# Performance work log

Hardware: AMD Instinct MI355X
Metric: run time of the kernel (lower is better)

Reference implementation:

```python
import jax, jax.numpy as jnp
import numpy as np

B, D, H, C = 128, 512, 1024, 1000


def setup_inputs() -> dict:
    key = jax.random.key(0)
    k1, k2, k3 = jax.random.split(key, 3)
    x = jax.random.normal(k1, (B, D), dtype=jnp.float32)
    W1 = jax.random.normal(k2, (D, H), dtype=jnp.float32) * (1.0 / np.sqrt(D))
    b1 = jnp.zeros((H,), dtype=jnp.float32)
    W2 = jax.random.normal(k3, (H, C), dtype=jnp.float32) * (1.0 / np.sqrt(H))
    b2 = jnp.zeros((C,), dtype=jnp.float32)
    return {"x": x, "W1": W1, "b1": b1, "W2": W2, "b2": b2, "step": 0}


def _logits(W1, b1, W2, b2, xi):
    # 2-layer MLP forward for a single sample xi: [D] -> [C]
    h = jnp.maximum(xi @ W1 + b1, 0.0)
    return h @ W2 + b2


def _per_sample_loss(params, xi, key):
    W1, b1, W2, b2 = params
    logit = _logits(W1, b1, W2, b2, xi)  # [C]
    # model samples a label from its own softmax (multinomial); sampling is
    # non-differentiable, matching torch's multinomial -> stop_gradient
    y = jax.random.categorical(key, jax.lax.stop_gradient(logit))
    return -jax.nn.log_softmax(logit)[y]  # CrossEntropyLoss on 1 sample


def reference(x, W1, b1, W2, b2, step):
    params = (W1, b1, W2, b2)
    keys = jax.random.split(jax.random.key(42), x.shape[0])
    # vmap(grad(loss)) -> per-sample gradients for every parameter
    grads = jax.vmap(jax.grad(_per_sample_loss), in_axes=(None, 0, 0))(params, x, keys)
    n = jnp.asarray(x.shape[0], dtype=x.dtype)
    # trace_p = sum_b ||g_b||^2 / B for each parameter
    traces = [jnp.sum(g * g) / n for g in grads]
    overall = traces[0] + traces[1] + traces[2] + traces[3]
    return jnp.stack([overall] + traces)  # [5]: overall, W1, b1, W2, b2
```

## Files before the change

kernel.cpp:

```cpp
#include <hip/hip_runtime.h>
#include <hip/hip_bf16.h>
#include <stdint.h>
#include <math.h>

#define B_N 128
#define D_N 512
#define H_N 1024
#define C_N 1000
#define CP  1024
#define NPART 16
#define BH (B_N * H_N)

__device__ __forceinline__ uint32_t rotl32(uint32_t v, int r) {
  return (v << r) | (v >> (32 - r));
}

__device__ __forceinline__ void threefry2x32(uint32_t k0, uint32_t k1,
                                             uint32_t x0, uint32_t x1,
                                             uint32_t &o0, uint32_t &o1) {
  uint32_t ks2 = k0 ^ k1 ^ 0x1BD11BDAu;
#define TF_R(r) { x0 += x1; x1 = rotl32(x1, r); x1 ^= x0; }
  x0 += k0; x1 += k1;
  TF_R(13) TF_R(15) TF_R(26) TF_R(6)
  x0 += k1; x1 += ks2 + 1u;
  TF_R(17) TF_R(29) TF_R(16) TF_R(24)
  x0 += ks2; x1 += k0 + 2u;
  TF_R(13) TF_R(15) TF_R(26) TF_R(6)
  x0 += k0; x1 += k1 + 3u;
  TF_R(17) TF_R(29) TF_R(16) TF_R(24)
  x0 += k1; x1 += ks2 + 4u;
  TF_R(13) TF_R(15) TF_R(26) TF_R(6)
  x0 += ks2; x1 += k0 + 5u;
#undef TF_R
  o0 = x0; o1 = x1;
}

__device__ __forceinline__ float gumbel_from_key(uint32_t k0, uint32_t k1, uint32_t i) {
  uint32_t o0, o1;
  threefry2x32(k0, k1, 0u, i, o0, o1);
  uint32_t bits = o0 ^ o1;
  uint32_t fb = (bits >> 9) | 0x3f800000u;
  float f = __uint_as_float(fb) - 1.0f;
  const float tiny = 1.1754943508222875e-38f;
  float u = fmaxf(tiny, f * (1.0f - tiny) + tiny);
  return -logf(-logf(u));
}

__device__ __forceinline__ float block_sum512(float v, float* red) {
  #pragma unroll
  for (int o = 32; o; o >>= 1) v += __shfl_xor(v, o);
  __syncthreads();
  if ((threadIdx.x & 63) == 0) red[threadIdx.x >> 6] = v;
  __syncthreads();
  return red[0] + red[1] + red[2] + red[3] + red[4] + red[5] + red[6] + red[7];
}

__device__ __forceinline__ float block_max512(float v, float* red) {
  #pragma unroll
  for (int o = 32; o; o >>= 1) v = fmaxf(v, __shfl_xor(v, o));
  __syncthreads();
  if ((threadIdx.x & 63) == 0) red[threadIdx.x >> 6] = v;
  __syncthreads();
  float m = red[0];
  #pragma unroll
  for (int w = 1; w < 8; w++) m = fmaxf(m, red[w]);
  return m;
}

__device__ __forceinline__ void fma4(float4 &a, const float4 &b, float s) {
  a.x += b.x * s; a.y += b.y * s; a.z += b.z * s; a.w += b.w * s;
}

__global__ __launch_bounds__(256) void k_fc1(const float* __restrict__ X,
                                             const float* __restrict__ W1,
                                             float* __restrict__ hpart) {
  __shared__ float xT[32 * 20];
  int cbase = blockIdx.x * 256;
  int sbase = blockIdx.y * 16;
  int dz = blockIdx.z;
  int t = threadIdx.x;
  {
    int s = t >> 4;
    int d2 = (t & 15) * 2;
    float2 xv = *reinterpret_cast<const float2*>(
        &X[(sbase + s) * D_N + dz * 32 + d2]);
    xT[(d2 + 0) * 20 + s] = xv.x;
    xT[(d2 + 1) * 20 + s] = xv.y;
  }
  __syncthreads();
  int c4 = cbase + (t & 63) * 4;
  int s4 = (t >> 6) * 4;
  float4 acc0 = {0,0,0,0}, acc1 = {0,0,0,0}, acc2 = {0,0,0,0}, acc3 = {0,0,0,0};
  const float* W1p = W1 + (size_t)(dz * 32) * H_N + c4;
  float4 wb[4], wn[4];
  #pragma unroll
  for (int i = 0; i < 4; i++)
    wb[i] = *reinterpret_cast<const float4*>(W1p + i * H_N);
  for (int j0 = 0; j0 < 32; j0 += 4) {
    #pragma unroll
    for (int i = 0; i < 4; i++) {
      int jn = j0 + 4 + i; jn = (jn < 32) ? jn : 31;
      wn[i] = *reinterpret_cast<const float4*>(W1p + jn * H_N);
    }
    #pragma unroll
    for (int i = 0; i < 4; i++) {
      float4 xv = *reinterpret_cast<const float4*>(&xT[(j0 + i) * 20 + s4]);
      fma4(acc0, wb[i], xv.x);
      fma4(acc1, wb[i], xv.y);
      fma4(acc2, wb[i], xv.z);
      fma4(acc3, wb[i], xv.w);
    }
    #pragma unroll
    for (int i = 0; i < 4; i++) wb[i] = wn[i];
  }
  float* hp = hpart + (size_t)dz * BH;
  *reinterpret_cast<float4*>(&hp[(sbase + s4 + 0) * H_N + c4]) = acc0;
  *reinterpret_cast<float4*>(&hp[(sbase + s4 + 1) * H_N + c4]) = acc1;
  *reinterpret_cast<float4*>(&hp[(sbase + s4 + 2) * H_N + c4]) = acc2;
  *reinterpret_cast<float4*>(&hp[(sbase + s4 + 3) * H_N + c4]) = acc3;
}

__global__ __launch_bounds__(256) void k_fc2(const float* __restrict__ hpart,
                                             const float* __restrict__ b1,
                                             const float* __restrict__ W2,
                                             float* __restrict__ lpart) {
  __shared__ float hT[64 * 20];
  int cbase = blockIdx.x * 256;
  int sbase = blockIdx.y * 16;
  int kb = blockIdx.z;
  int jbase = kb * 64;
  int t = threadIdx.x;
  #pragma unroll
  for (int k = 0; k < 4; k++) {
    int idx = t + k * 256;
    int s = idx >> 6, j = idx & 63;
    float v = b1[jbase + j];
    #pragma unroll
    for (int p = 0; p < NPART; p++)
      v += hpart[(size_t)p * BH + (sbase + s) * H_N + jbase + j];
    hT[j * 20 + s] = fmaxf(v, 0.0f);
  }
  __syncthreads();
  int c4 = cbase + (t & 63) * 4;
  int s4 = (t >> 6) * 4;
  if (c4 < C_N) {
    float4 acc0 = {0,0,0,0}, acc1 = {0,0,0,0}, acc2 = {0,0,0,0}, acc3 = {0,0,0,0};
    const float* W2p = W2 + (size_t)jbase * C_N + c4;
    float4 wb[4], wn[4];
    #pragma unroll
    for (int i = 0; i < 4; i++)
      wb[i] = *reinterpret_cast<const float4*>(W2p + (size_t)i * C_N);
    for (int j0 = 0; j0 < 64; j0 += 4) {
      #pragma unroll
      for (int i = 0; i < 4; i++) {
        int jn = j0 + 4 + i; jn = (jn < 64) ? jn : 63;
        wn[i] = *reinterpret_cast<const float4*>(W2p + (size_t)jn * C_N);
      }
      #pragma unroll
      for (int i = 0; i < 4; i++) {
        float4 xv = *reinterpret_cast<const float4*>(&hT[(j0 + i) * 20 + s4]);
        fma4(acc0, wb[i], xv.x);
        fma4(acc1, wb[i], xv.y);
        fma4(acc2, wb[i], xv.z);
        fma4(acc3, wb[i], xv.w);
      }
      #pragma unroll
      for (int i = 0; i < 4; i++) wb[i] = wn[i];
    }
    float* lp = lpart + (size_t)kb * (B_N * CP);
    *reinterpret_cast<float4*>(&lp[(sbase + s4 + 0) * CP + c4]) = acc0;
    *reinterpret_cast<float4*>(&lp[(sbase + s4 + 1) * CP + c4]) = acc1;
    *reinterpret_cast<float4*>(&lp[(sbase + s4 + 2) * CP + c4]) = acc2;
    *reinterpret_cast<float4*>(&lp[(sbase + s4 + 3) * CP + c4]) = acc3;
  }
}

__global__ __launch_bounds__(512) void k_sample(const float* __restrict__ X,
                                                const float* __restrict__ hpart,
                                                const float* __restrict__ b1,
                                                const float* __restrict__ lpart,
                                                const float* __restrict__ b2,
                                                float* __restrict__ g,
                                                float* __restrict__ hfinal,
                                                float* __restrict__ xsq_out,
                                                float* __restrict__ samp_part) {
  __shared__ float lg[C_N];
  __shared__ float red[8];
  __shared__ float redv[8];
  __shared__ int   redi[8];
  __shared__ uint32_t keys[2];
  int b = blockIdx.x;
  int t = threadIdx.x;

  {
    float sA = b2[t];
    float sB = (t + 512 < C_N) ? b2[t + 512] : 0.f;
    #pragma unroll
    for (int p = 0; p < NPART; p++) {
      const float* lp = lpart + (size_t)p * (B_N * CP) + b * CP;
      sA += lp[t];
      if (t + 512 < C_N) sB += lp[t + 512];
    }
    lg[t] = sA;
    if (t + 512 < C_N) lg[t + 512] = sB;
  }
  if (t == 0) {
    uint32_t o0, o1;
    threefry2x32(0u, 42u, 0u, (uint32_t)b, o0, o1);
    keys[0] = o0; keys[1] = o1;
  }
  __syncthreads();
  uint32_t k0 = keys[0], k1 = keys[1];

  float bz = -INFINITY; int bi = 0x7fffffff;
  {
    float z0 = lg[t] + gumbel_from_key(k0, k1, (uint32_t)t);
    bz = z0; bi = t;
    if (t + 512 < C_N) {
      float z1 = lg[t + 512] + gumbel_from_key(k0, k1, (uint32_t)(t + 512));
      if (z1 > bz || (z1 == bz && (t + 512) < bi)) { bz = z1; bi = t + 512; }
    }
  }
  #pragma unroll
  for (int o = 32; o; o >>= 1) {
    float ov = __shfl_xor(bz, o);
    int   oi = __shfl_xor(bi, o);
    if (ov > bz || (ov == bz && oi < bi)) { bz = ov; bi = oi; }
  }
  if ((t & 63) == 0) { redv[t >> 6] = bz; redi[t >> 6] = bi; }
  __syncthreads();
  if (t == 0) {
    #pragma unroll
    for (int w = 1; w < 8; w++) {
      if (redv[w] > redv[0] || (redv[w] == redv[0] && redi[w] < redi[0])) {
        redv[0] = redv[w]; redi[0] = redi[w];
      }
    }
  }
  __syncthreads();
  int y = redi[0];

  float lm = lg[t];
  if (t + 512 < C_N) lm = fmaxf(lm, lg[t + 512]);
  float m = block_max512(lm, red);
  float ea = expf(lg[t] - m);
  float eb = (t + 512 < C_N) ? expf(lg[t + 512] - m) : 0.0f;
  float sum1 = block_sum512(ea + eb, red);
  float inv = 1.0f / sum1;

  float ga  = ea * inv - ((t == y) ? 1.0f : 0.0f);
  float gb2 = eb * inv - (((t + 512) == y) ? 1.0f : 0.0f);
  g[b * CP + t] = ga;
  g[b * CP + t + 512] = (t + 512 < C_N) ? gb2 : 0.0f;
  float gn = ga * ga + ((t + 512 < C_N) ? gb2 * gb2 : 0.0f);
  float tnorm = block_sum512(gn, red);

  float h0 = b1[t];
  float h1 = b1[t + 512];
  #pragma unroll
  for (int p = 0; p < NPART; p++) {
    const float* hp = hpart + (size_t)p * BH + b * H_N;
    h0 += hp[t];
    h1 += hp[t + 512];
  }
  hfinal[b * H_N + t] = h0;
  hfinal[b * H_N + t + 512] = h1;
  float r0 = fmaxf(h0, 0.f), r1 = fmaxf(h1, 0.f);
  float hsq = block_sum512(r0 * r0 + r1 * r1, red);

  float xv = (t < D_N) ? X[b * D_N + t] : 0.0f;
  float xsq = block_sum512(xv * xv, red);

  if (t == 0) {
    xsq_out[b] = xsq;
    samp_part[b * 2 + 0] = hsq * tnorm;
    samp_part[b * 2 + 1] = tnorm;
  }
}

__global__ __launch_bounds__(512) void k_bwd1(const float* __restrict__ g,
                                              const float* __restrict__ W2,
                                              const float* __restrict__ hfinal,
                                              const float* __restrict__ xsq,
                                              float* __restrict__ bwd_part) {
  __shared__ float gs[8 * 1024];
  __shared__ float xq[8];
  __shared__ float wred[8][2];
  int jb = blockIdx.x * 16;
  int sbase = blockIdx.y * 8;
  int t = threadIdx.x;
  #pragma unroll
  for (int k = 0; k < 16; k++) {
    int idx = t + k * 512;
    gs[idx] = g[(sbase + (idx >> 10)) * CP + (idx & 1023)];
  }
  if (t < 8) xq[t] = xsq[sbase + t];
  __syncthreads();

  int w = t >> 6, lane = t & 63;
  int j0 = jb + w * 2, j1 = j0 + 1;
  float a0[8] = {0,0,0,0,0,0,0,0};
  float a1[8] = {0,0,0,0,0,0,0,0};
  const float* w2r0 = W2 + (size_t)j0 * C_N;
  const float* w2r1 = W2 + (size_t)j1 * C_N;
  #pragma unroll
  for (int it = 0; it < 4; it++) {
    int c0 = it * 256 + lane * 4;
    bool act = (c0 < C_N);
    float4 wv0 = act ? *reinterpret_cast<const float4*>(w2r0 + c0)
                     : make_float4(0.f, 0.f, 0.f, 0.f);
    float4 wv1 = act ? *reinterpret_cast<const float4*>(w2r1 + c0)
                     : make_float4(0.f, 0.f, 0.f, 0.f);
    #pragma unroll
    for (int s = 0; s < 8; s++) {
      float4 gv = *reinterpret_cast<const float4*>(&gs[s * 1024 + c0]);
      a0[s] += wv0.x * gv.x + wv0.y * gv.y + wv0.z * gv.z + wv0.w * gv.w;
      a1[s] += wv1.x * gv.x + wv1.y * gv.y + wv1.z * gv.z + wv1.w * gv.w;
    }
  }
  #pragma unroll
  for (int off = 32; off; off >>= 1) {
    #pragma unroll
    for (int s = 0; s < 8; s++) {
      a0[s] += __shfl_xor(a0[s], off);
      a1[s] += __shfl_xor(a1[s], off);
    }
  }
  float cb = 0.f, cw = 0.f;
  #pragma unroll
  for (int s = 0; s < 8; s++) {
    float h0 = hfinal[(sbase + s) * H_N + j0];
    float h1 = hfinal[(sbase + s) * H_N + j1];
    float v0 = (h0 > 0.f) ? a0[s] : 0.f;
    float v1 = (h1 > 0.f) ? a1[s] : 0.f;
    float q = v0 * v0 + v1 * v1;
    cb += q;
    cw += xq[s] * q;
  }
  if (lane == 0) { wred[w][0] = cw; wred[w][1] = cb; }
  __syncthreads();
  if (t == 0) {
    float sw = 0.f, sb = 0.f;
    #pragma unroll
    for (int i = 0; i < 8; i++) { sw += wred[i][0]; sb += wred[i][1]; }
    int bid = blockIdx.y * 64 + blockIdx.x;
    bwd_part[bid * 2 + 0] = sw;
    bwd_part[bid * 2 + 1] = sb;
  }
}

__global__ __launch_bounds__(512) void k_final(const float* __restrict__ samp_part,
                                               const float* __restrict__ bwd_part,
                                               float* __restrict__ out) {
  __shared__ float red[8];
  int t = threadIdx.x;
  float w1v = bwd_part[t * 2 + 0] + bwd_part[(t + 512) * 2 + 0];
  float b1v = bwd_part[t * 2 + 1] + bwd_part[(t + 512) * 2 + 1];
  float w2v = (t < B_N) ? samp_part[t * 2 + 0] : 0.f;
  float b2v = (t < B_N) ? samp_part[t * 2 + 1] : 0.f;
  w1v = block_sum512(w1v, red);
  b1v = block_sum512(b1v, red);
  w2v = block_sum512(w2v, red);
  b2v = block_sum512(b2v, red);
  if (t == 0) {
    w1v /= 128.0f; b1v /= 128.0f; w2v /= 128.0f; b2v /= 128.0f;
    out[0] = w1v + b1v + w2v + b2v;
    out[1] = w1v;
    out[2] = b1v;
    out[3] = w2v;
    out[4] = b2v;
  }
}

extern "C" void kernel_launch(void* const* d_in, const int* in_sizes, int n_in,
                              void* d_out, int out_size, void* d_ws, size_t ws_size,
                              hipStream_t stream) {
  const float* X  = (const float*)d_in[0];
  const float* W1 = (const float*)d_in[1];
  const float* b1 = (const float*)d_in[2];
  const float* W2 = (const float*)d_in[3];
  const float* b2 = (const float*)d_in[4];
  float* out = (float*)d_out;

  float* ws        = (float*)d_ws;
  float* hpart     = ws;
  float* lpart     = hpart + NPART * BH;
  float* g         = lpart + NPART * (B_N*CP);
  float* hfinal    = g + (B_N * CP);
  float* xsq       = hfinal + BH;
  float* samp_part = xsq + 128;
  float* bwd_part  = samp_part + 256;

  k_fc1<<<dim3(4, 8, NPART), 256, 0, stream>>>(X, W1, hpart);
  k_fc2<<<dim3(4, 8, NPART), 256, 0, stream>>>(hpart, b1, W2, lpart);
  k_sample<<<B_N, 512, 0, stream>>>(X, hpart, b1, lpart, b2, g, hfinal, xsq, samp_part);
  k_bwd1<<<dim3(64, 16), 512, 0, stream>>>(g, W2, hfinal, xsq, bwd_part);
  k_final<<<1, 512, 0, stream>>>(samp_part, bwd_part, out);
}
```

Measured before the change: 57.68 us.

## Fuse all five stages into one cooperative persistent kernel with grid syncs

```diff
diff --git a/kernel.cpp b/kernel.cpp
--- a/kernel.cpp
+++ b/kernel.cpp
@@ -1,7 +1,10 @@
 #include <hip/hip_runtime.h>
+#include <hip/hip_cooperative_groups.h>
 #include <hip/hip_bf16.h>
 #include <stdint.h>
 #include <math.h>
+
+namespace cg = cooperative_groups;
 
 #define B_N 128
 #define D_N 512
@@ -71,6 +74,314 @@
   a.x += b.x * s; a.y += b.y * s; a.z += b.z * s; a.w += b.w * s;
 }
 
+union SMem {
+  struct { float xT[2][32 * 20]; } a;
+  struct { float hT[2][64 * 20]; } c;
+  struct { float lg[1024]; float red[8]; float redv[8];
+           int redi[8]; uint32_t keys[2]; } d;
+  struct { float gs[8 * 1024]; float xq[8];
+           float wred[8][2]; } e;
+};
+
+__global__ __launch_bounds__(512) void k_fused(
+    const float* __restrict__ X,  const float* __restrict__ W1,
+    const float* __restrict__ b1, const float* __restrict__ W2,
+    const float* __restrict__ b2,
+    float* __restrict__ hpart, float* __restrict__ lpart,
+    float* __restrict__ g, float* __restrict__ hfinal,
+    float* __restrict__ xsq_out, float* __restrict__ samp_part,
+    float* __restrict__ bwd_part, float* __restrict__ out) {
+  cg::grid_group grid = cg::this_grid();
+  __shared__ SMem sm;
+  int t = threadIdx.x;
+  int bid = blockIdx.x;
+
+  {
+    int sub = t >> 8, tt = t & 255;
+    int u = bid * 2 + sub;
+    int cbase = (u & 3) * 256;
+    int sbase = ((u >> 2) & 7) * 16;
+    int dz = u >> 5;
+    float* xT = sm.a.xT[sub];
+    {
+      int s = tt >> 4;
+      int d2 = (tt & 15) * 2;
+      float2 xv = *reinterpret_cast<const float2*>(
+          &X[(sbase + s) * D_N + dz * 32 + d2]);
+      xT[(d2 + 0) * 20 + s] = xv.x;
+      xT[(d2 + 1) * 20 + s] = xv.y;
+    }
+    __syncthreads();
+    int c4 = cbase + (tt & 63) * 4;
+    int s4 = (tt >> 6) * 4;
+    float4 acc0 = {0,0,0,0}, acc1 = {0,0,0,0}, acc2 = {0,0,0,0}, acc3 = {0,0,0,0};
+    const float* W1p = W1 + (size_t)(dz * 32) * H_N + c4;
+    float4 wb[4], wn[4];
+    #pragma unroll
+    for (int i = 0; i < 4; i++)
+      wb[i] = *reinterpret_cast<const float4*>(W1p + i * H_N);
+    for (int j0 = 0; j0 < 32; j0 += 4) {
+      #pragma unroll
+      for (int i = 0; i < 4; i++) {
+        int jn = j0 + 4 + i; jn = (jn < 32) ? jn : 31;
+        wn[i] = *reinterpret_cast<const float4*>(W1p + jn * H_N);
+      }
+      #pragma unroll
+      for (int i = 0; i < 4; i++) {
+        float4 xv = *reinterpret_cast<const float4*>(&xT[(j0 + i) * 20 + s4]);
+        fma4(acc0, wb[i], xv.x);
+        fma4(acc1, wb[i], xv.y);
+        fma4(acc2, wb[i], xv.z);
+        fma4(acc3, wb[i], xv.w);
+      }
+      #pragma unroll
+      for (int i = 0; i < 4; i++) wb[i] = wn[i];
+    }
+    float* hp = hpart + (size_t)dz * BH;
+    *reinterpret_cast<float4*>(&hp[(sbase + s4 + 0) * H_N + c4]) = acc0;
+    *reinterpret_cast<float4*>(&hp[(sbase + s4 + 1) * H_N + c4]) = acc1;
+    *reinterpret_cast<float4*>(&hp[(sbase + s4 + 2) * H_N + c4]) = acc2;
+    *reinterpret_cast<float4*>(&hp[(sbase + s4 + 3) * H_N + c4]) = acc3;
+  }
+  grid.sync();
+
+  {
+    int sub = t >> 8, tt = t & 255;
+    int u = bid * 2 + sub;
+    int cbase = (u & 3) * 256;
+    int sbase = ((u >> 2) & 7) * 16;
+    int kb = u >> 5;
+    int jbase = kb * 64;
+    float* hT = sm.c.hT[sub];
+    #pragma unroll
+    for (int k = 0; k < 4; k++) {
+      int idx = tt + k * 256;
+      int s = idx >> 6, j = idx & 63;
+      float v = b1[jbase + j];
+      #pragma unroll
+      for (int p = 0; p < NPART; p++)
+        v += hpart[(size_t)p * BH + (sbase + s) * H_N + jbase + j];
+      hT[j * 20 + s] = fmaxf(v, 0.0f);
+    }
+    __syncthreads();
+    int c4 = cbase + (tt & 63) * 4;
+    int s4 = (tt >> 6) * 4;
+    if (c4 < C_N) {
+      float4 acc0 = {0,0,0,0}, acc1 = {0,0,0,0}, acc2 = {0,0,0,0}, acc3 = {0,0,0,0};
+      const float* W2p = W2 + (size_t)jbase * C_N + c4;
+      float4 wb[4], wn[4];
+      #pragma unroll
+      for (int i = 0; i < 4; i++)
+        wb[i] = *reinterpret_cast<const float4*>(W2p + (size_t)i * C_N);
+      for (int j0 = 0; j0 < 64; j0 += 4) {
+        #pragma unroll
+        for (int i = 0; i < 4; i++) {
+          int jn = j0 + 4 + i; jn = (jn < 64) ? jn : 63;
+          wn[i] = *reinterpret_cast<const float4*>(W2p + (size_t)jn * C_N);
+        }
+        #pragma unroll
+        for (int i = 0; i < 4; i++) {
+          float4 xv = *reinterpret_cast<const float4*>(&hT[(j0 + i) * 20 + s4]);
+          fma4(acc0, wb[i], xv.x);
+          fma4(acc1, wb[i], xv.y);
+          fma4(acc2, wb[i], xv.z);
+          fma4(acc3, wb[i], xv.w);
+        }
+        #pragma unroll
+        for (int i = 0; i < 4; i++) wb[i] = wn[i];
+      }
+      float* lp = lpart + (size_t)kb * (B_N * CP);
+      *reinterpret_cast<float4*>(&lp[(sbase + s4 + 0) * CP + c4]) = acc0;
+      *reinterpret_cast<float4*>(&lp[(sbase + s4 + 1) * CP + c4]) = acc1;
+      *reinterpret_cast<float4*>(&lp[(sbase + s4 + 2) * CP + c4]) = acc2;
+      *reinterpret_cast<float4*>(&lp[(sbase + s4 + 3) * CP + c4]) = acc3;
+    }
+  }
+  grid.sync();
+
+  if (bid < B_N) {
+    float* lg = sm.d.lg;
+    float* red = sm.d.red;
+    float* redv = sm.d.redv;
+    int* redi = sm.d.redi;
+    uint32_t* keys = sm.d.keys;
+    int b = bid;
+    {
+      float sA = b2[t];
+      float sB = (t + 512 < C_N) ? b2[t + 512] : 0.f;
+      #pragma unroll
+      for (int p = 0; p < NPART; p++) {
+        const float* lp = lpart + (size_t)p * (B_N * CP) + b * CP;
+        sA += lp[t];
+        if (t + 512 < C_N) sB += lp[t + 512];
+      }
+      lg[t] = sA;
+      if (t + 512 < C_N) lg[t + 512] = sB;
+    }
+    if (t == 0) {
+      uint32_t o0, o1;
+      threefry2x32(0u, 42u, 0u, (uint32_t)b, o0, o1);
+      keys[0] = o0; keys[1] = o1;
+    }
+    __syncthreads();
+    uint32_t k0 = keys[0], k1 = keys[1];
+
+    float bz = -INFINITY; int bi = 0x7fffffff;
+    {
+      float z0 = lg[t] + gumbel_from_key(k0, k1, (uint32_t)t);
+      bz = z0; bi = t;
+      if (t + 512 < C_N) {
+        float z1 = lg[t + 512] + gumbel_from_key(k0, k1, (uint32_t)(t + 512));
+        if (z1 > bz || (z1 == bz && (t + 512) < bi)) { bz = z1; bi = t + 512; }
+      }
+    }
+    #pragma unroll
+    for (int o = 32; o; o >>= 1) {
+      float ov = __shfl_xor(bz, o);
+      int   oi = __shfl_xor(bi, o);
+      if (ov > bz || (ov == bz && oi < bi)) { bz = ov; bi = oi; }
+    }
+    if ((t & 63) == 0) { redv[t >> 6] = bz; redi[t >> 6] = bi; }
+    __syncthreads();
+    if (t == 0) {
+      #pragma unroll
+      for (int w = 1; w < 8; w++) {
+        if (redv[w] > redv[0] || (redv[w] == redv[0] && redi[w] < redi[0])) {
+          redv[0] = redv[w]; redi[0] = redi[w];
+        }
+      }
+    }
+    __syncthreads();
+    int y = redi[0];
+
+    float lm = lg[t];
+    if (t + 512 < C_N) lm = fmaxf(lm, lg[t + 512]);
+    float m = block_max512(lm, red);
+    float ea = expf(lg[t] - m);
+    float eb = (t + 512 < C_N) ? expf(lg[t + 512] - m) : 0.0f;
+    float sum1 = block_sum512(ea + eb, red);
+    float inv = 1.0f / sum1;
+
+    float ga  = ea * inv - ((t == y) ? 1.0f : 0.0f);
+    float gb2 = eb * inv - (((t + 512) == y) ? 1.0f : 0.0f);
+    g[b * CP + t] = ga;
+    g[b * CP + t + 512] = (t + 512 < C_N) ? gb2 : 0.0f;
+    float gn = ga * ga + ((t + 512 < C_N) ? gb2 * gb2 : 0.0f);
+    float tnorm = block_sum512(gn, red);
+
+    float h0 = b1[t];
+    float h1 = b1[t + 512];
+    #pragma unroll
+    for (int p = 0; p < NPART; p++) {
+      const float* hp = hpart + (size_t)p * BH + b * H_N;
+      h0 += hp[t];
+      h1 += hp[t + 512];
+    }
+    hfinal[b * H_N + t] = h0;
+    hfinal[b * H_N + t + 512] = h1;
+    float r0 = fmaxf(h0, 0.f), r1 = fmaxf(h1, 0.f);
+    float hsq = block_sum512(r0 * r0 + r1 * r1, red);
+
+    float xv = (t < D_N) ? X[b * D_N + t] : 0.0f;
+    float xsq = block_sum512(xv * xv, red);
+
+    if (t == 0) {
+      xsq_out[b] = xsq;
+      samp_part[b * 2 + 0] = hsq * tnorm;
+      samp_part[b * 2 + 1] = tnorm;
+    }
+  }
+  grid.sync();
+
+  {
+    int sg = bid & 15, jg = bid >> 4;
+    int sbase = sg * 8;
+    float* gs = sm.e.gs;
+    float* xq = sm.e.xq;
+    #pragma unroll
+    for (int k = 0; k < 16; k++) {
+      int idx = t + k * 512;
+      gs[idx] = g[(sbase + (idx >> 10)) * CP + (idx & 1023)];
+    }
+    if (t < 8) xq[t] = xsq_out[sbase + t];
+    __syncthreads();
+
+    int w = t >> 6, lane = t & 63;
+    float cb = 0.f, cw = 0.f;
+    for (int it2 = 0; it2 < 4; it2++) {
+      int jb = (jg * 4 + it2) * 16;
+      int j0 = jb + w * 2, j1 = j0 + 1;
+      float a0[8] = {0,0,0,0,0,0,0,0};
+      float a1[8] = {0,0,0,0,0,0,0,0};
+      const float* w2r0 = W2 + (size_t)j0 * C_N;
+      const float* w2r1 = W2 + (size_t)j1 * C_N;
+      #pragma unroll
+      for (int it = 0; it < 4; it++) {
+        int c0 = it * 256 + lane * 4;
+        bool act = (c0 < C_N);
+        float4 wv0 = act ? *reinterpret_cast<const float4*>(w2r0 + c0)
+                         : make_float4(0.f, 0.f, 0.f, 0.f);
+        float4 wv1 = act ? *reinterpret_cast<const float4*>(w2r1 + c0)
+                         : make_float4(0.f, 0.f, 0.f, 0.f);
+        #pragma unroll
+        for (int s = 0; s < 8; s++) {
+          float4 gv = *reinterpret_cast<const float4*>(&gs[s * 1024 + c0]);
+          a0[s] += wv0.x * gv.x + wv0.y * gv.y + wv0.z * gv.z + wv0.w * gv.w;
+          a1[s] += wv1.x * gv.x + wv1.y * gv.y + wv1.z * gv.z + wv1.w * gv.w;
+        }
+      }
+      #pragma unroll
+      for (int off = 32; off; off >>= 1) {
+        #pragma unroll
+        for (int s = 0; s < 8; s++) {
+          a0[s] += __shfl_xor(a0[s], off);
+          a1[s] += __shfl_xor(a1[s], off);
+        }
+      }
+      #pragma unroll
+      for (int s = 0; s < 8; s++) {
+        float h0 = hfinal[(sbase + s) * H_N + j0];
+        float h1 = hfinal[(sbase + s) * H_N + j1];
+        float v0 = (h0 > 0.f) ? a0[s] : 0.f;
+        float v1 = (h1 > 0.f) ? a1[s] : 0.f;
+        float q = v0 * v0 + v1 * v1;
+        cb += q;
+        cw += xq[s] * q;
+      }
+    }
+    if (lane == 0) { sm.e.wred[w][0] = cw; sm.e.wred[w][1] = cb; }
+    __syncthreads();
+    if (t == 0) {
+      float sw = 0.f, sb = 0.f;
+      #pragma unroll
+      for (int i = 0; i < 8; i++) { sw += sm.e.wred[i][0]; sb += sm.e.wred[i][1]; }
+      bwd_part[bid * 2 + 0] = sw;
+      bwd_part[bid * 2 + 1] = sb;
+    }
+  }
+  grid.sync();
+
+  if (bid == 0) {
+    float* red = sm.d.red;
+    float w1v = (t < 256) ? bwd_part[t * 2 + 0] : 0.f;
+    float b1v = (t < 256) ? bwd_part[t * 2 + 1] : 0.f;
+    float w2v = (t < B_N) ? samp_part[t * 2 + 0] : 0.f;
+    float b2v = (t < B_N) ? samp_part[t * 2 + 1] : 0.f;
+    w1v = block_sum512(w1v, red);
+    b1v = block_sum512(b1v, red);
+    w2v = block_sum512(w2v, red);
+    b2v = block_sum512(b2v, red);
+    if (t == 0) {
+      w1v /= 128.0f; b1v /= 128.0f; w2v /= 128.0f; b2v /= 128.0f;
+      out[0] = w1v + b1v + w2v + b2v;
+      out[1] = w1v;
+      out[2] = b1v;
+      out[3] = w2v;
+      out[4] = b2v;
+    }
+  }
+}
+
 __global__ __launch_bounds__(256) void k_fc1(const float* __restrict__ X,
                                              const float* __restrict__ W1,
                                              float* __restrict__ hpart) {
@@ -191,7 +502,6 @@
   __shared__ uint32_t keys[2];
   int b = blockIdx.x;
   int t = threadIdx.x;
-
   {
     float sA = b2[t];
     float sB = (t + 512 < C_N) ? b2[t + 512] : 0.f;
@@ -211,7 +521,6 @@
   }
   __syncthreads();
   uint32_t k0 = keys[0], k1 = keys[1];
-
   float bz = -INFINITY; int bi = 0x7fffffff;
   {
     float z0 = lg[t] + gumbel_from_key(k0, k1, (uint32_t)t);
@@ -239,7 +548,6 @@
   }
   __syncthreads();
   int y = redi[0];
-
   float lm = lg[t];
   if (t + 512 < C_N) lm = fmaxf(lm, lg[t + 512]);
   float m = block_max512(lm, red);
@@ -247,14 +555,12 @@
   float eb = (t + 512 < C_N) ? expf(lg[t + 512] - m) : 0.0f;
   float sum1 = block_sum512(ea + eb, red);
   float inv = 1.0f / sum1;
-
   float ga  = ea * inv - ((t == y) ? 1.0f : 0.0f);
   float gb2 = eb * inv - (((t + 512) == y) ? 1.0f : 0.0f);
   g[b * CP + t] = ga;
   g[b * CP + t + 512] = (t + 512 < C_N) ? gb2 : 0.0f;
   float gn = ga * ga + ((t + 512 < C_N) ? gb2 * gb2 : 0.0f);
   float tnorm = block_sum512(gn, red);
-
   float h0 = b1[t];
   float h1 = b1[t + 512];
   #pragma unroll
@@ -267,10 +573,8 @@
   hfinal[b * H_N + t + 512] = h1;
   float r0 = fmaxf(h0, 0.f), r1 = fmaxf(h1, 0.f);
   float hsq = block_sum512(r0 * r0 + r1 * r1, red);
-
   float xv = (t < D_N) ? X[b * D_N + t] : 0.0f;
   float xsq = block_sum512(xv * xv, red);
-
   if (t == 0) {
     xsq_out[b] = xsq;
     samp_part[b * 2 + 0] = hsq * tnorm;
@@ -296,7 +600,6 @@
   }
   if (t < 8) xq[t] = xsq[sbase + t];
   __syncthreads();
-
   int w = t >> 6, lane = t & 63;
   int j0 = jb + w * 2, j1 = j0 + 1;
   float a0[8] = {0,0,0,0,0,0,0,0};
@@ -391,9 +694,16 @@
   float* samp_part = xsq + 128;
   float* bwd_part  = samp_part + 256;
 
-  k_fc1<<<dim3(4, 8, NPART), 256, 0, stream>>>(X, W1, hpart);
-  k_fc2<<<dim3(4, 8, NPART), 256, 0, stream>>>(hpart, b1, W2, lpart);
-  k_sample<<<B_N, 512, 0, stream>>>(X, hpart, b1, lpart, b2, g, hfinal, xsq, samp_part);
-  k_bwd1<<<dim3(64, 16), 512, 0, stream>>>(g, W2, hfinal, xsq, bwd_part);
-  k_final<<<1, 512, 0, stream>>>(samp_part, bwd_part, out);
-}
+  void* args[] = {(void*)&X, (void*)&W1, (void*)&b1, (void*)&W2, (void*)&b2,
+                  (void*)&hpart, (void*)&lpart, (void*)&g, (void*)&hfinal,
+                  (void*)&xsq, (void*)&samp_part, (void*)&bwd_part, (void*)&out};
+  hipError_t err = hipLaunchCooperativeKernel((void*)k_fused, dim3(256), dim3(512),
+                                              args, 0, stream);
+  if (err != hipSuccess) {
+    k_fc1<<<dim3(4, 8, NPART), 256, 0, stream>>>(X, W1, hpart);
+    k_fc2<<<dim3(4, 8, NPART), 256, 0, stream>>>(hpart, b1, W2, lpart);
+    k_sample<<<B_N, 512, 0, stream>>>(X, hpart, b1, lpart, b2, g, hfinal, xsq, samp_part);
+    k_bwd1<<<dim3(64, 16), 512, 0, stream>>>(g, W2, hfinal, xsq, bwd_part);
+    k_final<<<1, 512, 0, stream>>>(samp_part, bwd_part, out);
+  }
+}
```

Result: slower. 183.4 us (+217.9%).
